# Optimization experiments

Hardware: AMD Instinct MI355X
Metric: run time of the kernel (lower is better)

## Reference

```python
import jax, jax.numpy as jnp
import numpy as np

EPS = 1e-7
NCE_T = 0.07
NCE_M = 0.5

def _unit(x):
    return x / jnp.sqrt(jnp.sum(x * x, axis=-1, keepdims=True))

def setup_inputs() -> dict:
    key = jax.random.key(0)
    k1, k2, k3, k4, k5, k6 = jax.random.split(key, 6)
    B, D, K, N = 256, 128, 8192, 500000
    f_s = _unit(jax.random.normal(k1, (B, D), dtype=jnp.float32))
    f_t = _unit(jax.random.normal(k2, (B, D), dtype=jnp.float32))
    memory_v1 = _unit(jax.random.normal(k3, (N, D), dtype=jnp.float32))
    memory_v2 = _unit(jax.random.normal(k4, (N, D), dtype=jnp.float32))
    idx = jax.random.randint(k5, (B,), 0, N)
    contrast_idx = jax.random.randint(k6, (B, K), 0, N)
    return {"f_s": f_s, "f_t": f_t, "memory_v1": memory_v1,
            "memory_v2": memory_v2, "idx": idx, "contrast_idx": contrast_idx}

def _contrast_loss(x, n_data):
    # ContrastLoss (Eq 18): x is [B, K+1], col 0 = positive score
    bsz = x.shape[0]
    m = x.shape[1] - 1
    Pn = 1.0 / float(n_data)
    denom_add = m * Pn + EPS
    log_D1 = jnp.log(x[:, 0] / (x[:, 0] + denom_add))          # positives
    log_D0 = jnp.log((m * Pn) / (x[:, 1:] + denom_add))        # negatives
    return -(log_D1.sum() + log_D0.sum()) / bsz

def reference(f_s, f_t, memory_v1, memory_v2, idx, contrast_idx):
    n_data = memory_v1.shape[0]
    # full index set: positive in column 0, then K negatives
    full_idx = jnp.concatenate([idx[:, None], contrast_idx], axis=1)  # [B, K+1]
    # gather memory rows (detached in the original torch code)
    w_v1 = jax.lax.stop_gradient(memory_v1[full_idx])  # [B, K+1, D]
    w_v2 = jax.lax.stop_gradient(memory_v2[full_idx])  # [B, K+1, D]
    # per-sample dot-product scoring + temperature
    out_v2 = jnp.exp(jnp.einsum('bkd,bd->bk', w_v1, f_t) / NCE_T)
    out_v1 = jnp.exp(jnp.einsum('bkd,bd->bk', w_v2, f_s) / NCE_T)
    # Z set on first forward as mean * outputSize (a detached scalar in torch)
    Z_v1 = jax.lax.stop_gradient(out_v1.mean()) * n_data
    Z_v2 = jax.lax.stop_gradient(out_v2.mean()) * n_data
    out_v1 = out_v1 / Z_v1
    out_v2 = out_v2 / Z_v2
    # momentum scatter update of memory banks (no-grad in original)
    def update(mem, feats):
        old = mem[idx]                                   # [B, D]
        new = old * NCE_M + feats * (1.0 - NCE_M)
        new = new / jnp.sqrt(jnp.sum(new * new, axis=1, keepdims=True))
        return mem.at[idx].set(new)
    new_v1 = update(memory_v1, jax.lax.stop_gradient(f_s))
    new_v2 = update(memory_v2, jax.lax.stop_gradient(f_t))
    # out_s = out_v1 (student anchored), out_t = out_v2 (teacher anchored)
    loss = _contrast_loss(out_v1, n_data) + _contrast_loss(out_v2, n_data)
    return loss, new_v1, new_v2
```

## Files before the change

kernel.cpp:

```cpp
#include <hip/hip_runtime.h>
#include <stdint.h>

#define BB   256
#define DD   128
#define KK   8192
#define KP1  8193
#define NDATA 500000
#define MEMELEMS 64000000

__global__ __launch_bounds__(256) void score_kernel(
    const float* __restrict__ f_s, const float* __restrict__ f_t,
    const float* __restrict__ mv1, const float* __restrict__ mv2,
    const int* __restrict__ idx, const int* __restrict__ cidx,
    float* __restrict__ sA, float* __restrict__ sB, double* __restrict__ acc)
{
    const int b   = blockIdx.y;
    const int tid = threadIdx.x;
    const int g   = tid >> 4;
    const int fl  = tid & 15;

    const float4* fs4 = (const float4*)f_s;
    const float4* ft4 = (const float4*)f_t;
    const float4* m14 = (const float4*)mv1;
    const float4* m24 = (const float4*)mv2;

    const int foff = b * 32 + fl * 2;
    const float4 fsa = fs4[foff], fsb = fs4[foff + 1];
    const float4 fta = ft4[foff], ftb = ft4[foff + 1];

    const float invT = 1.0f / 0.07f;
    float accA = 0.f, accB = 0.f;
    const int kbase = blockIdx.x * 128;

    #pragma unroll
    for (int it = 0; it < 8; ++it) {
        const int k = kbase + it * 16 + g;
        if (k < KP1) {
            const int j  = (k == 0) ? idx[b] : cidx[b * KK + (k - 1)];
            const int ro = j * 32 + fl * 2;
            const float4 a1 = m14[ro], b1 = m14[ro + 1];
            const float4 a2 = m24[ro], b2 = m24[ro + 1];
            float p1 = a2.x*fsa.x + a2.y*fsa.y + a2.z*fsa.z + a2.w*fsa.w
                     + b2.x*fsb.x + b2.y*fsb.y + b2.z*fsb.z + b2.w*fsb.w;
            float p2 = a1.x*fta.x + a1.y*fta.y + a1.z*fta.z + a1.w*fta.w
                     + b1.x*ftb.x + b1.y*ftb.y + b1.z*ftb.z + b1.w*ftb.w;
            #pragma unroll
            for (int off = 1; off < 16; off <<= 1) {
                p1 += __shfl_xor(p1, off);
                p2 += __shfl_xor(p2, off);
            }
            if (fl == 0) {
                const float e1 = __expf(p1 * invT);
                const float e2 = __expf(p2 * invT);
                sA[b * KP1 + k] = e1;
                sB[b * KP1 + k] = e2;
                accA += e1;
                accB += e2;
            }
        }
    }

    __shared__ float lA[16], lB[16];
    if (fl == 0) { lA[g] = accA; lB[g] = accB; }
    __syncthreads();
    if (tid == 0) {
        float ta = 0.f, tb = 0.f;
        #pragma unroll
        for (int i = 0; i < 16; ++i) { ta += lA[i]; tb += lB[i]; }
        atomicAdd(&acc[0], (double)ta);
        atomicAdd(&acc[1], (double)tb);
    }
}

__global__ __launch_bounds__(256) void loss_kernel(
    const float* __restrict__ sA, const float* __restrict__ sB,
    const double* __restrict__ acc, double* __restrict__ lossAcc)
{
    const int b = blockIdx.y;
    const int k = blockIdx.x * 256 + threadIdx.x;

    const double denom = (double)BB * (double)KP1;
    const float invZ1 = (float)(denom / (acc[0] * (double)NDATA));
    const float invZ2 = (float)(denom / (acc[1] * (double)NDATA));
    const float mPn = (float)KK / (float)NDATA;
    const float c   = mPn + 1e-7f;

    float t = 0.f;
    if (k < KP1) {
        const float x1 = sA[b * KP1 + k] * invZ1;
        const float x2 = sB[b * KP1 + k] * invZ2;
        if (k == 0) {
            t = logf(x1 / (x1 + c)) + logf(x2 / (x2 + c));
        } else {
            t = logf(mPn / (x1 + c)) + logf(mPn / (x2 + c));
        }
    }
    #pragma unroll
    for (int off = 1; off < 64; off <<= 1) t += __shfl_xor(t, off);
    __shared__ float ls[4];
    if ((threadIdx.x & 63) == 0) ls[threadIdx.x >> 6] = t;
    __syncthreads();
    if (threadIdx.x == 0)
        atomicAdd(lossAcc, (double)(ls[0] + ls[1] + ls[2] + ls[3]));
}

__global__ void finalize_kernel(const double* __restrict__ acc,
                                float* __restrict__ out)
{
    out[0] = (float)(-acc[2] / (double)BB);
}

__global__ __launch_bounds__(128) void update_kernel(
    const float* __restrict__ mv1, const float* __restrict__ mv2,
    const float* __restrict__ f_s, const float* __restrict__ f_t,
    const int* __restrict__ idx, float* __restrict__ out)
{
    const int v = blockIdx.x >> 8;
    const int b = blockIdx.x & 255;
    const int j = idx[b];
    for (int b2 = b + 1; b2 < BB; ++b2)
        if (idx[b2] == j) return;

    const float* mem = v ? mv2 : mv1;
    const float* f   = v ? f_t : f_s;
    const int t = threadIdx.x;
    const float n = 0.5f * mem[(size_t)j * DD + t] + 0.5f * f[b * DD + t];

    float ss = n * n;
    #pragma unroll
    for (int off = 1; off < 64; off <<= 1) ss += __shfl_xor(ss, off);
    __shared__ float ls[2];
    if ((t & 63) == 0) ls[t >> 6] = ss;
    __syncthreads();
    const float total = ls[0] + ls[1];

    out[1 + (size_t)v * MEMELEMS + (size_t)j * DD + t] = n / sqrtf(total);
}

extern "C" void kernel_launch(void* const* d_in, const int* in_sizes, int n_in,
                              void* d_out, int out_size, void* d_ws, size_t ws_size,
                              hipStream_t stream)
{
    const float* f_s = (const float*)d_in[0];
    const float* f_t = (const float*)d_in[1];
    const float* mv1 = (const float*)d_in[2];
    const float* mv2 = (const float*)d_in[3];
    const int*   idx  = (const int*)d_in[4];
    const int*   cidx = (const int*)d_in[5];
    float* out = (float*)d_out;

    const size_t sElems = (size_t)BB * KP1;
    double* acc;
    float*  sA;
    if (ws_size >= 256 + 2 * sElems * sizeof(float)) {
        acc = (double*)d_ws;
        sA  = (float*)((char*)d_ws + 256);
    } else {
        uintptr_t p = (uintptr_t)(out + 1 + (size_t)MEMELEMS);
        p = (p + 255) & ~(uintptr_t)255;
        acc = (double*)p;
        sA  = (float*)(acc + 8);
    }
    float* sB = sA + sElems;

    hipMemsetAsync(acc, 0, 3 * sizeof(double), stream);

    dim3 gS(65, BB);
    score_kernel<<<gS, 256, 0, stream>>>(f_s, f_t, mv1, mv2, idx, cidx, sA, sB, acc);

    dim3 gL(33, BB);
    loss_kernel<<<gL, 256, 0, stream>>>(sA, sB, acc, &acc[2]);

    finalize_kernel<<<1, 1, 0, stream>>>(acc, out);

    hipMemcpyAsync(out + 1, mv1, (size_t)MEMELEMS * sizeof(float),
                   hipMemcpyDeviceToDevice, stream);
    hipMemcpyAsync(out + 1 + (size_t)MEMELEMS, mv2, (size_t)MEMELEMS * sizeof(float),
                   hipMemcpyDeviceToDevice, stream);
    update_kernel<<<512, 128, 0, stream>>>(mv1, mv2, f_s, f_t, idx, out);
}
```

Measured before the change: 1.577 ms.

## Split positive/negative scoring with batched gathers and replace memcpy with copy kernel

```diff
diff --git a/kernel.cpp b/kernel.cpp
--- a/kernel.cpp
+++ b/kernel.cpp
@@ -8,10 +8,10 @@
 #define NDATA 500000
 #define MEMELEMS 64000000
 
-__global__ __launch_bounds__(256) void score_kernel(
+__global__ __launch_bounds__(256) void score_neg_kernel(
     const float* __restrict__ f_s, const float* __restrict__ f_t,
     const float* __restrict__ mv1, const float* __restrict__ mv2,
-    const int* __restrict__ idx, const int* __restrict__ cidx,
+    const int* __restrict__ cidx,
     float* __restrict__ sA, float* __restrict__ sB, double* __restrict__ acc)
 {
     const int b   = blockIdx.y;
@@ -28,40 +28,102 @@
     const float4 fsa = fs4[foff], fsb = fs4[foff + 1];
     const float4 fta = ft4[foff], ftb = ft4[foff + 1];
 
+    const int s0 = blockIdx.x * 64 + g;
+
+    int j[4];
+    #pragma unroll
+    for (int it = 0; it < 4; ++it)
+        j[it] = cidx[b * KK + s0 + it * 16];
+
+    float4 a1[4], b1[4], a2[4], b2[4];
+    #pragma unroll
+    for (int it = 0; it < 4; ++it) {
+        const int ro = j[it] * 32 + fl * 2;
+        a1[it] = m14[ro]; b1[it] = m14[ro + 1];
+        a2[it] = m24[ro]; b2[it] = m24[ro + 1];
+    }
+
     const float invT = 1.0f / 0.07f;
     float accA = 0.f, accB = 0.f;
-    const int kbase = blockIdx.x * 128;
-
-    #pragma unroll
-    for (int it = 0; it < 8; ++it) {
-        const int k = kbase + it * 16 + g;
-        if (k < KP1) {
-            const int j  = (k == 0) ? idx[b] : cidx[b * KK + (k - 1)];
-            const int ro = j * 32 + fl * 2;
-            const float4 a1 = m14[ro], b1 = m14[ro + 1];
-            const float4 a2 = m24[ro], b2 = m24[ro + 1];
-            float p1 = a2.x*fsa.x + a2.y*fsa.y + a2.z*fsa.z + a2.w*fsa.w
-                     + b2.x*fsb.x + b2.y*fsb.y + b2.z*fsb.z + b2.w*fsb.w;
-            float p2 = a1.x*fta.x + a1.y*fta.y + a1.z*fta.z + a1.w*fta.w
-                     + b1.x*ftb.x + b1.y*ftb.y + b1.z*ftb.z + b1.w*ftb.w;
-            #pragma unroll
-            for (int off = 1; off < 16; off <<= 1) {
-                p1 += __shfl_xor(p1, off);
-                p2 += __shfl_xor(p2, off);
-            }
-            if (fl == 0) {
-                const float e1 = __expf(p1 * invT);
-                const float e2 = __expf(p2 * invT);
-                sA[b * KP1 + k] = e1;
-                sB[b * KP1 + k] = e2;
-                accA += e1;
-                accB += e2;
-            }
+
+    #pragma unroll
+    for (int it = 0; it < 4; ++it) {
+        float p1 = a2[it].x*fsa.x + a2[it].y*fsa.y + a2[it].z*fsa.z + a2[it].w*fsa.w
+                 + b2[it].x*fsb.x + b2[it].y*fsb.y + b2[it].z*fsb.z + b2[it].w*fsb.w;
+        float p2 = a1[it].x*fta.x + a1[it].y*fta.y + a1[it].z*fta.z + a1[it].w*fta.w
+                 + b1[it].x*ftb.x + b1[it].y*ftb.y + b1[it].z*ftb.z + b1[it].w*ftb.w;
+        #pragma unroll
+        for (int off = 1; off < 16; off <<= 1) {
+            p1 += __shfl_xor(p1, off);
+            p2 += __shfl_xor(p2, off);
+        }
+        if (fl == 0) {
+            const int k = s0 + it * 16 + 1;
+            const float e1 = __expf(p1 * invT);
+            const float e2 = __expf(p2 * invT);
+            sA[b * KP1 + k] = e1;
+            sB[b * KP1 + k] = e2;
+            accA += e1;
+            accB += e2;
         }
     }
 
     __shared__ float lA[16], lB[16];
     if (fl == 0) { lA[g] = accA; lB[g] = accB; }
+    __syncthreads();
+    if (tid == 0) {
+        float ta = 0.f, tb = 0.f;
+        #pragma unroll
+        for (int i = 0; i < 16; ++i) { ta += lA[i]; tb += lB[i]; }
+        atomicAdd(&acc[0], (double)ta);
+        atomicAdd(&acc[1], (double)tb);
+    }
+}
+
+__global__ __launch_bounds__(256) void score_pos_kernel(
+    const float* __restrict__ f_s, const float* __restrict__ f_t,
+    const float* __restrict__ mv1, const float* __restrict__ mv2,
+    const int* __restrict__ idx,
+    float* __restrict__ sA, float* __restrict__ sB, double* __restrict__ acc)
+{
+    const int tid = threadIdx.x;
+    const int g   = tid >> 4;
+    const int fl  = tid & 15;
+    const int b   = blockIdx.x * 16 + g;
+
+    const float4* fs4 = (const float4*)f_s;
+    const float4* ft4 = (const float4*)f_t;
+    const float4* m14 = (const float4*)mv1;
+    const float4* m24 = (const float4*)mv2;
+
+    const int foff = b * 32 + fl * 2;
+    const float4 fsa = fs4[foff], fsb = fs4[foff + 1];
+    const float4 fta = ft4[foff], ftb = ft4[foff + 1];
+
+    const int j  = idx[b];
+    const int ro = j * 32 + fl * 2;
+    const float4 a1 = m14[ro], b1 = m14[ro + 1];
+    const float4 a2 = m24[ro], b2 = m24[ro + 1];
+
+    float p1 = a2.x*fsa.x + a2.y*fsa.y + a2.z*fsa.z + a2.w*fsa.w
+             + b2.x*fsb.x + b2.y*fsb.y + b2.z*fsb.z + b2.w*fsb.w;
+    float p2 = a1.x*fta.x + a1.y*fta.y + a1.z*fta.z + a1.w*fta.w
+             + b1.x*ftb.x + b1.y*ftb.y + b1.z*ftb.z + b1.w*ftb.w;
+    #pragma unroll
+    for (int off = 1; off < 16; off <<= 1) {
+        p1 += __shfl_xor(p1, off);
+        p2 += __shfl_xor(p2, off);
+    }
+
+    __shared__ float lA[16], lB[16];
+    const float invT = 1.0f / 0.07f;
+    if (fl == 0) {
+        const float e1 = __expf(p1 * invT);
+        const float e2 = __expf(p2 * invT);
+        sA[(size_t)b * KP1] = e1;
+        sB[(size_t)b * KP1] = e2;
+        lA[g] = e1; lB[g] = e2;
+    }
     __syncthreads();
     if (tid == 0) {
         float ta = 0.f, tb = 0.f;
@@ -108,6 +170,18 @@
                                 float* __restrict__ out)
 {
     out[0] = (float)(-acc[2] / (double)BB);
+}
+
+__global__ __launch_bounds__(256) void copy_kernel(
+    const float4* __restrict__ mv1, const float4* __restrict__ mv2,
+    float4* __restrict__ o1, float4* __restrict__ o2)
+{
+    const size_t n4 = (size_t)MEMELEMS / 4;
+    const size_t stride = (size_t)gridDim.x * 256;
+    for (size_t i = (size_t)blockIdx.x * 256 + threadIdx.x; i < n4; i += stride) {
+        o1[i] = mv1[i];
+        o2[i] = mv2[i];
+    }
 }
 
 __global__ __launch_bounds__(128) void update_kernel(
@@ -165,17 +239,16 @@
 
     hipMemsetAsync(acc, 0, 3 * sizeof(double), stream);
 
-    dim3 gS(65, BB);
-    score_kernel<<<gS, 256, 0, stream>>>(f_s, f_t, mv1, mv2, idx, cidx, sA, sB, acc);
+    dim3 gN(128, BB);
+    score_neg_kernel<<<gN, 256, 0, stream>>>(f_s, f_t, mv1, mv2, cidx, sA, sB, acc);
+    score_pos_kernel<<<16, 256, 0, stream>>>(f_s, f_t, mv1, mv2, idx, sA, sB, acc);
 
     dim3 gL(33, BB);
     loss_kernel<<<gL, 256, 0, stream>>>(sA, sB, acc, &acc[2]);
-
     finalize_kernel<<<1, 1, 0, stream>>>(acc, out);
 
-    hipMemcpyAsync(out + 1, mv1, (size_t)MEMELEMS * sizeof(float),
-                   hipMemcpyDeviceToDevice, stream);
-    hipMemcpyAsync(out + 1 + (size_t)MEMELEMS, mv2, (size_t)MEMELEMS * sizeof(float),
-                   hipMemcpyDeviceToDevice, stream);
+    copy_kernel<<<8192, 256, 0, stream>>>(
+        (const float4*)mv1, (const float4*)mv2,
+        (float4*)(out + 1), (float4*)(out + 1 + (size_t)MEMELEMS));
     update_kernel<<<512, 128, 0, stream>>>(mv1, mv2, f_s, f_t, idx, out);
 }
```

New measurement: 1.771 ms. 1.12x slower.
